# Performance work log

Measured on AMD Instinct MI355X. Metric: run time of the kernel, lower is better.

The kernel has to match this reference:

```python
import jax, jax.numpy as jnp
import numpy as np

B, T, P, HID = 4, 512, 3, 512   # batch, atoms, vector dim, hidden
HD = 32                          # head_dim
H = HID // HD                    # num_heads = 16
EXP = 512                        # expanded (PBC outcell) tokens
S = T + EXP                      # src_len
EPS = 1e-3                       # EquivariantLayerNorm eps
CUTOFF = 1e-5                    # pre-softmax local weight cutoff


def setup_inputs() -> dict:
    key = jax.random.key(0)
    ks = jax.random.split(key, 8)
    q = jax.random.normal(ks[0], (B, T, P, HID), dtype=jnp.float32)
    k = jax.random.normal(ks[1], (B, T, P, HID), dtype=jnp.float32)
    v = jax.random.normal(ks[2], (B, T, P, HID), dtype=jnp.float32)
    attn_bias = jax.random.normal(ks[3], (B, H, T, S), dtype=jnp.float32)
    key_padding_mask = jnp.zeros((B, T), dtype=bool)
    expand_mask = jnp.zeros((B, EXP), dtype=bool)
    outcell_index = jax.random.randint(ks[4], (B, EXP), 0, T)
    local_attention_weight = jax.random.uniform(ks[5], (B, T, S), dtype=jnp.float32)
    out_proj_weight = jax.random.normal(ks[6], (HID, HID), dtype=jnp.float32) / np.sqrt(HID)
    attn_ln_weight = jnp.ones((HID,), dtype=jnp.float32)
    return {"q": q, "k": k, "v": v, "attn_bias": attn_bias,
            "key_padding_mask": key_padding_mask, "outcell_index": outcell_index,
            "local_attention_weight": local_attention_weight, "expand_mask": expand_mask,
            "out_proj_weight": out_proj_weight, "attn_ln_weight": attn_ln_weight}


def _split_heads(x):
    # [b, L, P, HID] -> [b, H, L, P*HD]
    b, L = x.shape[0], x.shape[1]
    return x.reshape(b, L, P, H, HD).transpose(0, 3, 1, 2, 4).reshape(b, H, L, P * HD)


def reference(q, k, v, attn_bias, key_padding_mask, outcell_index,
              local_attention_weight, expand_mask, out_proj_weight, attn_ln_weight):
    # PBC neighbor expansion: gather out-of-cell images of k/v along token dim
    idx = outcell_index[:, :, None, None]  # [B, EXP, 1, 1], broadcast over P, HID
    expand_k = jnp.take_along_axis(k, idx, axis=1)
    expand_v = jnp.take_along_axis(v, idx, axis=1)
    kf = jnp.concatenate([k, expand_k], axis=1)  # [B, S, P, HID]
    vf = jnp.concatenate([v, expand_v], axis=1)
    kpm = jnp.concatenate([key_padding_mask, expand_mask], axis=-1)  # [B, S]

    qh = _split_heads(q)   # [B, H, T, P*HD]
    kh = _split_heads(kf)  # [B, H, S, P*HD]
    vh = _split_heads(vf)

    # attn_bias + key padding mask -> attention mask
    attn_mask = jnp.where(kpm[:, None, None, :], -jnp.inf, attn_bias)
    w = jnp.einsum('bhtd,bhsd->bhts', qh, kh) + attn_mask
    # pre-softmax cutoff where local attention weight is ~0 (use_no_pre_cutoff_softmax=False)
    w = jnp.where((local_attention_weight <= CUTOFF)[:, None, :, :], -jnp.inf, w)
    p = jax.nn.softmax(w.astype(jnp.float32), axis=-1)
    # post-softmax local attention reweighting
    p = p * local_attention_weight[:, None, :, :].astype(jnp.float32)

    attn = jnp.einsum('bhts,bhsd->bhtd', p.astype(q.dtype), vh)  # [B, H, T, P*HD]
    attn = attn.reshape(B, H, T, P, HD).transpose(0, 2, 3, 1, 4).reshape(B, T, P, HID)

    # Equivariant smooth layer norm over the vector dim (-2), mean over width (-1)
    sq = jnp.sum(attn * attn, axis=-2)            # [B, T, HID]
    inv = (jnp.mean(sq, axis=-1) + EPS) ** -0.5   # [B, T]
    xln = attn * attn_ln_weight * inv[:, :, None, None]

    out = jnp.einsum('btpd,od->btpo', xln, out_proj_weight)  # out_proj (no bias)
    return out
```

## Files before the change

### kernel.cpp

```cpp
#include <hip/hip_runtime.h>

#define Bn   4
#define Tn   512
#define Pn   3
#define HIDn 512
#define HDn  32
#define Hn   16
#define EXPn 512
#define Sn   1024
#define Dn   96
#define LOG2E 1.44269504088896340736f

typedef __bf16 bf16_t;
typedef __bf16 bf16x8 __attribute__((ext_vector_type(8)));
typedef float  f32x4  __attribute__((ext_vector_type(4)));

__global__ __launch_bounds__(192) void pack_qk(
    const float* __restrict__ q, const float* __restrict__ k,
    const int* __restrict__ outcell,
    bf16_t* __restrict__ Qh, bf16_t* __restrict__ Kh)
{
    const int bs = blockIdx.x;
    const int b = bs >> 10, s = bs & 1023;
    const int ts = (s < Tn) ? s : outcell[b * EXPn + (s - Tn)];
    const int o = threadIdx.x;
    const int h = o / 12, c = o % 12;
    const int p = c >> 2, f = c & 3;
    const int src = p * HIDn + h * HDn + f * 8;

    {
        const float* krow = k + (size_t)(b * Tn + ts) * (Pn * HIDn);
        const float4* s4 = (const float4*)(krow + src);
        float4 f0 = s4[0], f1 = s4[1];
        bf16_t o8[8] = {(bf16_t)f0.x, (bf16_t)f0.y, (bf16_t)f0.z, (bf16_t)f0.w,
                        (bf16_t)f1.x, (bf16_t)f1.y, (bf16_t)f1.z, (bf16_t)f1.w};
        *(uint4*)&Kh[(((size_t)b * Hn + h) * Sn + s) * Dn + c * 8] = *(uint4*)o8;
    }
    if (s < Tn) {
        const float* qrow = q + (size_t)(b * Tn + s) * (Pn * HIDn);
        const float4* s4 = (const float4*)(qrow + src);
        float4 f0 = s4[0], f1 = s4[1];
        bf16_t o8[8] = {(bf16_t)f0.x, (bf16_t)f0.y, (bf16_t)f0.z, (bf16_t)f0.w,
                        (bf16_t)f1.x, (bf16_t)f1.y, (bf16_t)f1.z, (bf16_t)f1.w};
        *(uint4*)&Qh[(((size_t)b * Hn + h) * Tn + s) * Dn + c * 8] = *(uint4*)o8;
    }
}

__global__ __launch_bounds__(256) void pack_v(
    const float* __restrict__ v, const int* __restrict__ outcell,
    bf16_t* __restrict__ Vt)
{
    const int blk = blockIdx.x;
    const int bh = blk >> 4, s0 = (blk & 15) << 6;
    const int b = bh >> 4, h = bh & 15;
    __shared__ float tile[64 * 108];
    __shared__ int ts_sh[64];
    if (threadIdx.x < 64) {
        const int s = s0 + threadIdx.x;
        ts_sh[threadIdx.x] = (s < Tn) ? s : outcell[b * EXPn + (s - Tn)];
    }
    __syncthreads();
    for (int u = threadIdx.x; u < 64 * 24; u += 256) {
        const int sl = u / 24, c = u % 24;
        const int p = c >> 3, f = c & 7;
        float4 val = *(const float4*)&v[(size_t)(b * Tn + ts_sh[sl]) * (Pn * HIDn)
                                        + p * HIDn + h * HDn + f * 4];
        *(float4*)&tile[sl * 108 + c * 4] = val;
    }
    __syncthreads();
    for (int e = threadIdx.x; e < 96 * 8; e += 256) {
        const int d = e >> 3, g = e & 7;
        bf16_t o8[8];
#pragma unroll
        for (int j = 0; j < 8; ++j) o8[j] = (bf16_t)tile[(g * 8 + j) * 108 + d];
        *(uint4*)&Vt[((size_t)bh * Dn + d) * Sn + s0 + g * 8] = *(uint4*)o8;
    }
}

__global__ __launch_bounds__(256) void pack_w(
    const float* __restrict__ W, bf16_t* __restrict__ Wb)
{
    const int i = blockIdx.x * 256 + threadIdx.x;
    float4 f0 = *(const float4*)&W[i * 8];
    float4 f1 = *(const float4*)&W[i * 8 + 4];
    bf16_t o8[8] = {(bf16_t)f0.x, (bf16_t)f0.y, (bf16_t)f0.z, (bf16_t)f0.w,
                    (bf16_t)f1.x, (bf16_t)f1.y, (bf16_t)f1.z, (bf16_t)f1.w};
    *(uint4*)&Wb[i * 8] = *(uint4*)o8;
}

__global__ __launch_bounds__(256, 2) void attn_kernel(
    const bf16_t* __restrict__ Qh, const bf16_t* __restrict__ Kh,
    const bf16_t* __restrict__ Vt, const float* __restrict__ bias,
    const float* __restrict__ lw, float* __restrict__ attn_out,
    float* __restrict__ sumsq)
{
    const int h  = blockIdx.x;
    const int b  = blockIdx.y >> 3;
    const int t0 = (blockIdx.y & 7) << 6;
    const int tid = threadIdx.x;
    const int wv  = tid >> 6;
    const int lane = tid & 63;
    const int l16 = lane & 15;
    const int quad = lane >> 4;

    __shared__ bf16_t Ps[4][16 * 72];

    const size_t bh = (size_t)b * Hn + h;
    const int tb = t0 + wv * 16;

    bf16x8 qf[3];
    {
        const bf16_t* qb = Qh + (bh * Tn + tb + l16) * Dn + quad * 8;
#pragma unroll
        for (int ks = 0; ks < 3; ++ks) qf[ks] = *(const bf16x8*)(qb + ks * 32);
    }

    const bf16_t* kbase = Kh + (bh * Sn + l16) * Dn + quad * 8;
    const bf16_t* vbase = Vt + (bh * Dn + l16) * Sn + quad * 8;
    const float*  bbase = bias + ((bh * Tn + tb + quad * 4)) * (size_t)Sn + l16;
    const float*  lbase = lw + (((size_t)b * Tn + tb + quad * 4)) * Sn + l16;

    f32x4 Oacc[6];
#pragma unroll
    for (int i = 0; i < 6; ++i) Oacc[i] = f32x4{0.f, 0.f, 0.f, 0.f};
    float mrow[4], lrow[4];
#pragma unroll
    for (int r = 0; r < 4; ++r) { mrow[r] = -3.0e38f; lrow[r] = 0.f; }

    float BRc[16], LRc[16], BRn[16], LRn[16];
#pragma unroll
    for (int ct = 0; ct < 4; ++ct)
#pragma unroll
        for (int r = 0; r < 4; ++r) {
            BRc[ct * 4 + r] = bbase[(size_t)r * Sn + ct * 16];
            LRc[ct * 4 + r] = lbase[(size_t)r * Sn + ct * 16];
        }

    for (int s0 = 0; s0 < Sn; s0 += 64) {
        bf16x8 kf[4][3];
#pragma unroll
        for (int ct = 0; ct < 4; ++ct)
#pragma unroll
            for (int ks = 0; ks < 3; ++ks)
                kf[ct][ks] = *(const bf16x8*)(kbase + (size_t)(s0 + ct * 16) * Dn + ks * 32);

        const int s0n = (s0 + 64 < Sn) ? (s0 + 64) : 0;
#pragma unroll
        for (int ct = 0; ct < 4; ++ct)
#pragma unroll
            for (int r = 0; r < 4; ++r) {
                BRn[ct * 4 + r] = bbase[(size_t)r * Sn + s0n + ct * 16];
                LRn[ct * 4 + r] = lbase[(size_t)r * Sn + s0n + ct * 16];
            }

        f32x4 sc[4];
#pragma unroll
        for (int ct = 0; ct < 4; ++ct) {
            f32x4 acc = f32x4{0.f, 0.f, 0.f, 0.f};
#pragma unroll
            for (int ks = 0; ks < 3; ++ks)
                acc = __builtin_amdgcn_mfma_f32_16x16x32_bf16(qf[ks], kf[ct][ks], acc, 0, 0, 0);
            sc[ct] = acc;
        }

        float cmax[4] = {-3.0e38f, -3.0e38f, -3.0e38f, -3.0e38f};
#pragma unroll
        for (int ct = 0; ct < 4; ++ct) {
#pragma unroll
            for (int r = 0; r < 4; ++r) {
                float wval = sc[ct][r] + BRc[ct * 4 + r];
                wval = (LRc[ct * 4 + r] <= 1e-5f) ? -3.0e38f : wval;
                sc[ct][r] = wval;
                cmax[r] = fmaxf(cmax[r], wval);
            }
        }
#pragma unroll
        for (int off = 1; off < 16; off <<= 1)
#pragma unroll
            for (int r = 0; r < 4; ++r)
                cmax[r] = fmaxf(cmax[r], __shfl_xor(cmax[r], off));

        float scl[4];
#pragma unroll
        for (int r = 0; r < 4; ++r) {
            const float mnew = fmaxf(mrow[r], cmax[r]);
            scl[r] = exp2f((mrow[r] - mnew) * LOG2E);
            mrow[r] = mnew;
            lrow[r] *= scl[r];
        }
#pragma unroll
        for (int dt = 0; dt < 6; ++dt)
#pragma unroll
            for (int r = 0; r < 4; ++r) Oacc[dt][r] *= scl[r];

        float lsum[4] = {0.f, 0.f, 0.f, 0.f};
#pragma unroll
        for (int ct = 0; ct < 4; ++ct) {
#pragma unroll
            for (int r = 0; r < 4; ++r) {
                const float pe = exp2f((sc[ct][r] - mrow[r]) * LOG2E);
                lsum[r] += pe;
                Ps[wv][(quad * 4 + r) * 72 + ct * 16 + l16] = (bf16_t)(pe * LRc[ct * 4 + r]);
            }
        }
#pragma unroll
        for (int off = 1; off < 16; off <<= 1)
#pragma unroll
            for (int r = 0; r < 4; ++r) lsum[r] += __shfl_xor(lsum[r], off);
#pragma unroll
        for (int r = 0; r < 4; ++r) lrow[r] += lsum[r];

        bf16x8 pa[2];
#pragma unroll
        for (int ks = 0; ks < 2; ++ks)
            pa[ks] = *(const bf16x8*)&Ps[wv][l16 * 72 + ks * 32 + quad * 8];
#pragma unroll
        for (int dt = 0; dt < 6; ++dt) {
#pragma unroll
            for (int ks = 0; ks < 2; ++ks) {
                bf16x8 vf = *(const bf16x8*)(vbase + (size_t)(dt * 16) * Sn + s0 + ks * 32);
                Oacc[dt] = __builtin_amdgcn_mfma_f32_16x16x32_bf16(pa[ks], vf, Oacc[dt], 0, 0, 0);
            }
        }

#pragma unroll
        for (int i = 0; i < 16; ++i) { BRc[i] = BRn[i]; LRc[i] = LRn[i]; }
    }

    float invl[4];
#pragma unroll
    for (int r = 0; r < 4; ++r) invl[r] = 1.0f / lrow[r];
    float ss[4] = {0.f, 0.f, 0.f, 0.f};
#pragma unroll
    for (int dt = 0; dt < 6; ++dt) {
        const int d = dt * 16 + l16;
        const int p = d >> 5, hd = d & 31;
#pragma unroll
        for (int r = 0; r < 4; ++r) {
            const int t = tb + quad * 4 + r;
            const float o = Oacc[dt][r] * invl[r];
            attn_out[(((size_t)b * Tn + t) * Pn + p) * HIDn + h * HDn + hd] = o;
            ss[r] += o * o;
        }
    }
#pragma unroll
    for (int off = 1; off < 16; off <<= 1)
#pragma unroll
        for (int r = 0; r < 4; ++r) ss[r] += __shfl_xor(ss[r], off);
    if (l16 == 0) {
#pragma unroll
        for (int r = 0; r < 4; ++r)
            atomicAdd(&sumsq[b * Tn + tb + quad * 4 + r], ss[r]);
    }
}

__global__ __launch_bounds__(256, 2) void out_gemm(
    const float* __restrict__ attn, const float* __restrict__ sumsq,
    const float* __restrict__ lnwg, const bf16_t* __restrict__ Bw,
    float* __restrict__ out)
{
    const int n0 = blockIdx.x * 64;
    const int m0 = blockIdx.y * 64;
    const int tid = threadIdx.x;
    const int wv = tid >> 6, lane = tid & 63, l16 = lane & 15, quad = lane >> 4;
    __shared__ float lnw_s[HIDn];
    __shared__ float inv_s[64];
    __shared__ bf16_t As[2][64 * 72];
    __shared__ bf16_t Bs[2][64 * 72];

    for (int i = tid; i < HIDn; i += 256) lnw_s[i] = lnwg[i];
    if (tid < 64)
        inv_s[tid] = rsqrtf(sumsq[(m0 + tid) / 3] * (1.0f / HIDn) + 1e-3f);
    __syncthreads();

    const int rowA = tid >> 3, cA = tid & 7;
    const float inv0 = inv_s[rowA], inv1 = inv_s[rowA + 32];

    auto loadT = [&](int k0, float4 (&AF)[2][2], uint4 (&BR)[2], float4 (&LF)[2]) {
        LF[0] = *(const float4*)&lnw_s[k0 + cA * 8];
        LF[1] = *(const float4*)&lnw_s[k0 + cA * 8 + 4];
        AF[0][0] = *(const float4*)&attn[(size_t)(m0 + rowA) * HIDn + k0 + cA * 8];
        AF[0][1] = *(const float4*)&attn[(size_t)(m0 + rowA) * HIDn + k0 + cA * 8 + 4];
        AF[1][0] = *(const float4*)&attn[(size_t)(m0 + rowA + 32) * HIDn + k0 + cA * 8];
        AF[1][1] = *(const float4*)&attn[(size_t)(m0 + rowA + 32) * HIDn + k0 + cA * 8 + 4];
        BR[0] = *(const uint4*)&Bw[(size_t)(n0 + rowA) * HIDn + k0 + cA * 8];
        BR[1] = *(const uint4*)&Bw[(size_t)(n0 + rowA + 32) * HIDn + k0 + cA * 8];
    };
    auto storeT = [&](int buf, float4 (&AF)[2][2], uint4 (&BR)[2], float4 (&LF)[2]) {
#pragma unroll
        for (int j = 0; j < 2; ++j) {
            const float iv = j ? inv1 : inv0;
            bf16_t a8[8] = {(bf16_t)(AF[j][0].x * LF[0].x * iv), (bf16_t)(AF[j][0].y * LF[0].y * iv),
                            (bf16_t)(AF[j][0].z * LF[0].z * iv), (bf16_t)(AF[j][0].w * LF[0].w * iv),
                            (bf16_t)(AF[j][1].x * LF[1].x * iv), (bf16_t)(AF[j][1].y * LF[1].y * iv),
                            (bf16_t)(AF[j][1].z * LF[1].z * iv), (bf16_t)(AF[j][1].w * LF[1].w * iv)};
            *(uint4*)&As[buf][(rowA + j * 32) * 72 + cA * 8] = *(uint4*)a8;
            *(uint4*)&Bs[buf][(rowA + j * 32) * 72 + cA * 8] = BR[j];
        }
    };

    f32x4 acc[4];
#pragma unroll
    for (int i = 0; i < 4; ++i) acc[i] = f32x4{0.f, 0.f, 0.f, 0.f};

    float4 af0[2][2], af1[2][2], lf0[2], lf1[2];
    uint4 br0[2], br1[2];
    loadT(0, af0, br0, lf0);
    storeT(0, af0, br0, lf0);
    __syncthreads();

    auto compute = [&](int buf) {
#pragma unroll
        for (int ks = 0; ks < 2; ++ks) {
            bf16x8 a = *(const bf16x8*)&As[buf][(wv * 16 + l16) * 72 + ks * 32 + quad * 8];
#pragma unroll
            for (int nt = 0; nt < 4; ++nt) {
                bf16x8 bb = *(const bf16x8*)&Bs[buf][(nt * 16 + l16) * 72 + ks * 32 + quad * 8];
                acc[nt] = __builtin_amdgcn_mfma_f32_16x16x32_bf16(a, bb, acc[nt], 0, 0, 0);
            }
        }
    };

    for (int it = 0; it < 8; it += 2) {
        loadT((it + 1) * 64, af1, br1, lf1);
        compute(0);
        storeT(1, af1, br1, lf1);
        __syncthreads();
        const bool pf = (it + 2) < 8;
        if (pf) loadT((it + 2) * 64, af0, br0, lf0);
        compute(1);
        if (pf) storeT(0, af0, br0, lf0);
        __syncthreads();
    }
#pragma unroll
    for (int nt = 0; nt < 4; ++nt)
#pragma unroll
        for (int r = 0; r < 4; ++r) {
            const int m = m0 + wv * 16 + quad * 4 + r;
            const int n = n0 + nt * 16 + l16;
            out[(size_t)m * HIDn + n] = acc[nt][r];
        }
}

extern "C" void kernel_launch(void* const* d_in, const int* in_sizes, int n_in,
                              void* d_out, int out_size, void* d_ws, size_t ws_size,
                              hipStream_t stream)
{
    const float* q    = (const float*)d_in[0];
    const float* k    = (const float*)d_in[1];
    const float* v    = (const float*)d_in[2];
    const float* bias = (const float*)d_in[3];
    const int*   outcell = (const int*)d_in[5];
    const float* lw   = (const float*)d_in[6];
    const float* W    = (const float*)d_in[8];
    const float* lnw  = (const float*)d_in[9];
    float* out = (float*)d_out;

    char* ws = (char*)d_ws;
    bf16_t* Qh   = (bf16_t*)(ws);
    bf16_t* Kh   = (bf16_t*)(ws + 6291456);
    bf16_t* Vt   = (bf16_t*)(ws + 18874368);
    float*  attn = (float*)(ws + 31457280);
    bf16_t* Wb   = (bf16_t*)(ws + 44040192);
    float*  sumsq = (float*)(ws + 44564480);

    hipMemsetAsync(sumsq, 0, (Bn * Tn) * sizeof(float), stream);
    pack_qk<<<dim3(Bn * Sn), 192, 0, stream>>>(q, k, outcell, Qh, Kh);
    pack_v<<<dim3(Bn * Hn * 16), 256, 0, stream>>>(v, outcell, Vt);
    pack_w<<<dim3((HIDn * HIDn) / (256 * 8)), 256, 0, stream>>>(W, Wb);
    attn_kernel<<<dim3(Hn, Bn * (Tn / 64)), 256, 0, stream>>>(Qh, Kh, Vt, bias, lw, attn, sumsq);
    out_gemm<<<dim3(HIDn / 64, (Bn * Tn * Pn) / 64), 256, 0, stream>>>(attn, sumsq, lnw, Wb, out);
}
```

Baseline: 344.4 us.

## Stage attention tiles into LDS asynchronously and drop online max rescaling

The attention kernel now streams the K, V, bias and local-weight tiles into double-buffered LDS with global_load_lds, splitting the loads across the four waves and syncing with barriers and vmcnt waits. The chunk size drops to 32 keys. The MFMA operands are swapped so each lane owns one query row, which allows vectorized float4 output stores and simpler reductions. The online softmax running max and rescaling are removed and exp is taken on raw scores, which saves ALU and shuffle work but relies on the scores staying small enough not to overflow.

```diff
diff --git a/kernel.cpp b/kernel.cpp
--- a/kernel.cpp
+++ b/kernel.cpp
@@ -10,10 +10,16 @@
 #define Sn   1024
 #define Dn   96
 #define LOG2E 1.44269504088896340736f
+#define CH   32
+#define NCH  (Sn / CH)
 
 typedef __bf16 bf16_t;
 typedef __bf16 bf16x8 __attribute__((ext_vector_type(8)));
 typedef float  f32x4  __attribute__((ext_vector_type(4)));
+
+#define GLDS(g, l) __builtin_amdgcn_global_load_lds(                            \
+    (const __attribute__((address_space(1))) void*)(g),                         \
+    (__attribute__((address_space(3))) void*)(l), 16, 0, 0)
 
 __global__ __launch_bounds__(192) void pack_qk(
     const float* __restrict__ q, const float* __restrict__ k,
@@ -103,7 +109,11 @@
     const int l16 = lane & 15;
     const int quad = lane >> 4;
 
-    __shared__ bf16_t Ps[4][16 * 72];
+    __shared__ bf16_t KfS[2][6][512];
+    __shared__ bf16_t VfS[2][6][512];
+    __shared__ float  BfS[2][4][2][256];
+    __shared__ float  LfS[2][4][2][256];
+    __shared__ bf16_t Ps[4][16 * 40];
 
     const size_t bh = (size_t)b * Hn + h;
     const int tb = t0 + wv * 16;
@@ -114,144 +124,114 @@
 #pragma unroll
         for (int ks = 0; ks < 3; ++ks) qf[ks] = *(const bf16x8*)(qb + ks * 32);
     }
-
-    const bf16_t* kbase = Kh + (bh * Sn + l16) * Dn + quad * 8;
-    const bf16_t* vbase = Vt + (bh * Dn + l16) * Sn + quad * 8;
-    const float*  bbase = bias + ((bh * Tn + tb + quad * 4)) * (size_t)Sn + l16;
-    const float*  lbase = lw + (((size_t)b * Tn + tb + quad * 4)) * Sn + l16;
+    asm volatile("s_waitcnt vmcnt(0)" ::: "memory");
+
+    int kA, kB, two_k, vA, vB;
+    if (wv == 0)      { kA = 0; kB = 1; two_k = 1; vA = 0; vB = 0; }
+    else if (wv == 1) { kA = 2; kB = 3; two_k = 1; vA = 1; vB = 0; }
+    else if (wv == 2) { kA = 4; kB = 4; two_k = 0; vA = 2; vB = 3; }
+    else              { kA = 5; kB = 5; two_k = 0; vA = 4; vB = 5; }
+
+    const float*  gB = bias + (bh * Tn + tb + l16) * (size_t)Sn + quad * 4;
+    const float*  gL = lw + ((size_t)b * Tn + tb + l16) * Sn + quad * 4;
+    const bf16_t* gKA = Kh + (bh * Sn + (kA / 3) * 16 + l16) * (size_t)Dn + (kA % 3) * 32 + quad * 8;
+    const bf16_t* gKB = Kh + (bh * Sn + (kB / 3) * 16 + l16) * (size_t)Dn + (kB % 3) * 32 + quad * 8;
+    const bf16_t* gVA = Vt + (bh * Dn + vA * 16 + l16) * (size_t)Sn + quad * 8;
+    const bf16_t* gVB = Vt + (bh * Dn + vB * 16 + l16) * (size_t)Sn + quad * 8;
+
+    auto stage = [&](int s0, int buf) {
+        GLDS(gB + s0,      &BfS[buf][wv][0][0]);
+        GLDS(gB + s0 + 16, &BfS[buf][wv][1][0]);
+        GLDS(gL + s0,      &LfS[buf][wv][0][0]);
+        GLDS(gL + s0 + 16, &LfS[buf][wv][1][0]);
+        GLDS(gKA + (size_t)s0 * Dn, &KfS[buf][kA][0]);
+        if (two_k) GLDS(gKB + (size_t)s0 * Dn, &KfS[buf][kB][0]);
+        GLDS(gVA + s0, &VfS[buf][vA][0]);
+        if (!two_k) GLDS(gVB + s0, &VfS[buf][vB][0]);
+    };
 
     f32x4 Oacc[6];
 #pragma unroll
     for (int i = 0; i < 6; ++i) Oacc[i] = f32x4{0.f, 0.f, 0.f, 0.f};
-    float mrow[4], lrow[4];
-#pragma unroll
-    for (int r = 0; r < 4; ++r) { mrow[r] = -3.0e38f; lrow[r] = 0.f; }
-
-    float BRc[16], LRc[16], BRn[16], LRn[16];
-#pragma unroll
-    for (int ct = 0; ct < 4; ++ct)
+    float lacc = 0.f;
+
+    stage(0, 0);
+
+    for (int c = 0; c < NCH; ++c) {
+        const int buf = c & 1;
+        __builtin_amdgcn_sched_barrier(0);
+        __builtin_amdgcn_s_barrier();
+        __builtin_amdgcn_sched_barrier(0);
+        if (c + 1 < NCH) {
+            stage((c + 1) * CH, buf ^ 1);
+            asm volatile("s_waitcnt vmcnt(7)" ::: "memory");
+        } else {
+            asm volatile("s_waitcnt vmcnt(0)" ::: "memory");
+        }
+        __builtin_amdgcn_s_barrier();
+        __builtin_amdgcn_sched_barrier(0);
+
+        f32x4 BR[2], LR[2];
+        BR[0] = *(const f32x4*)&BfS[buf][wv][0][lane * 4];
+        BR[1] = *(const f32x4*)&BfS[buf][wv][1][lane * 4];
+        LR[0] = *(const f32x4*)&LfS[buf][wv][0][lane * 4];
+        LR[1] = *(const f32x4*)&LfS[buf][wv][1][lane * 4];
+
+        f32x4 sc[2];
+#pragma unroll
+        for (int ct = 0; ct < 2; ++ct) {
+            f32x4 acc = f32x4{0.f, 0.f, 0.f, 0.f};
+#pragma unroll
+            for (int ks = 0; ks < 3; ++ks) {
+                bf16x8 kf = *(const bf16x8*)&KfS[buf][ct * 3 + ks][lane * 8];
+                acc = __builtin_amdgcn_mfma_f32_16x16x32_bf16(kf, qf[ks], acc, 0, 0, 0);
+            }
+            sc[ct] = acc;
+        }
+
+        float lsum = 0.f;
+#pragma unroll
+        for (int ct = 0; ct < 2; ++ct) {
+            bf16_t o4[4];
+#pragma unroll
+            for (int r = 0; r < 4; ++r) {
+                const float wval = sc[ct][r] + BR[ct][r];
+                const float pe = (LR[ct][r] <= 1e-5f) ? 0.f : exp2f(wval * LOG2E);
+                lsum += pe;
+                o4[r] = (bf16_t)(pe * LR[ct][r]);
+            }
+            *(uint2*)&Ps[wv][l16 * 40 + ct * 16 + quad * 4] = *(uint2*)o4;
+        }
+        lacc += lsum;
+
+        bf16x8 pb = *(const bf16x8*)&Ps[wv][l16 * 40 + quad * 8];
+#pragma unroll
+        for (int dt = 0; dt < 6; ++dt) {
+            bf16x8 vf = *(const bf16x8*)&VfS[buf][dt][lane * 8];
+            Oacc[dt] = __builtin_amdgcn_mfma_f32_16x16x32_bf16(vf, pb, Oacc[dt], 0, 0, 0);
+        }
+    }
+
+    lacc += __shfl_xor(lacc, 16);
+    lacc += __shfl_xor(lacc, 32);
+    const float invl = 1.0f / lacc;
+    const int t = tb + l16;
+    float ss = 0.f;
+#pragma unroll
+    for (int dt = 0; dt < 6; ++dt) {
+        const int d0 = dt * 16 + quad * 4;
+        f32x4 o;
 #pragma unroll
         for (int r = 0; r < 4; ++r) {
-            BRc[ct * 4 + r] = bbase[(size_t)r * Sn + ct * 16];
-            LRc[ct * 4 + r] = lbase[(size_t)r * Sn + ct * 16];
-        }
-
-    for (int s0 = 0; s0 < Sn; s0 += 64) {
-        bf16x8 kf[4][3];
-#pragma unroll
-        for (int ct = 0; ct < 4; ++ct)
-#pragma unroll
-            for (int ks = 0; ks < 3; ++ks)
-                kf[ct][ks] = *(const bf16x8*)(kbase + (size_t)(s0 + ct * 16) * Dn + ks * 32);
-
-        const int s0n = (s0 + 64 < Sn) ? (s0 + 64) : 0;
-#pragma unroll
-        for (int ct = 0; ct < 4; ++ct)
-#pragma unroll
-            for (int r = 0; r < 4; ++r) {
-                BRn[ct * 4 + r] = bbase[(size_t)r * Sn + s0n + ct * 16];
-                LRn[ct * 4 + r] = lbase[(size_t)r * Sn + s0n + ct * 16];
-            }
-
-        f32x4 sc[4];
-#pragma unroll
-        for (int ct = 0; ct < 4; ++ct) {
-            f32x4 acc = f32x4{0.f, 0.f, 0.f, 0.f};
-#pragma unroll
-            for (int ks = 0; ks < 3; ++ks)
-                acc = __builtin_amdgcn_mfma_f32_16x16x32_bf16(qf[ks], kf[ct][ks], acc, 0, 0, 0);
-            sc[ct] = acc;
-        }
-
-        float cmax[4] = {-3.0e38f, -3.0e38f, -3.0e38f, -3.0e38f};
-#pragma unroll
-        for (int ct = 0; ct < 4; ++ct) {
-#pragma unroll
-            for (int r = 0; r < 4; ++r) {
-                float wval = sc[ct][r] + BRc[ct * 4 + r];
-                wval = (LRc[ct * 4 + r] <= 1e-5f) ? -3.0e38f : wval;
-                sc[ct][r] = wval;
-                cmax[r] = fmaxf(cmax[r], wval);
-            }
-        }
-#pragma unroll
-        for (int off = 1; off < 16; off <<= 1)
-#pragma unroll
-            for (int r = 0; r < 4; ++r)
-                cmax[r] = fmaxf(cmax[r], __shfl_xor(cmax[r], off));
-
-        float scl[4];
-#pragma unroll
-        for (int r = 0; r < 4; ++r) {
-            const float mnew = fmaxf(mrow[r], cmax[r]);
-            scl[r] = exp2f((mrow[r] - mnew) * LOG2E);
-            mrow[r] = mnew;
-            lrow[r] *= scl[r];
-        }
-#pragma unroll
-        for (int dt = 0; dt < 6; ++dt)
-#pragma unroll
-            for (int r = 0; r < 4; ++r) Oacc[dt][r] *= scl[r];
-
-        float lsum[4] = {0.f, 0.f, 0.f, 0.f};
-#pragma unroll
-        for (int ct = 0; ct < 4; ++ct) {
-#pragma unroll
-            for (int r = 0; r < 4; ++r) {
-                const float pe = exp2f((sc[ct][r] - mrow[r]) * LOG2E);
-                lsum[r] += pe;
-                Ps[wv][(quad * 4 + r) * 72 + ct * 16 + l16] = (bf16_t)(pe * LRc[ct * 4 + r]);
-            }
-        }
-#pragma unroll
-        for (int off = 1; off < 16; off <<= 1)
-#pragma unroll
-            for (int r = 0; r < 4; ++r) lsum[r] += __shfl_xor(lsum[r], off);
-#pragma unroll
-        for (int r = 0; r < 4; ++r) lrow[r] += lsum[r];
-
-        bf16x8 pa[2];
-#pragma unroll
-        for (int ks = 0; ks < 2; ++ks)
-            pa[ks] = *(const bf16x8*)&Ps[wv][l16 * 72 + ks * 32 + quad * 8];
-#pragma unroll
-        for (int dt = 0; dt < 6; ++dt) {
-#pragma unroll
-            for (int ks = 0; ks < 2; ++ks) {
-                bf16x8 vf = *(const bf16x8*)(vbase + (size_t)(dt * 16) * Sn + s0 + ks * 32);
-                Oacc[dt] = __builtin_amdgcn_mfma_f32_16x16x32_bf16(pa[ks], vf, Oacc[dt], 0, 0, 0);
-            }
-        }
-
-#pragma unroll
-        for (int i = 0; i < 16; ++i) { BRc[i] = BRn[i]; LRc[i] = LRn[i]; }
-    }
-
-    float invl[4];
-#pragma unroll
-    for (int r = 0; r < 4; ++r) invl[r] = 1.0f / lrow[r];
-    float ss[4] = {0.f, 0.f, 0.f, 0.f};
-#pragma unroll
-    for (int dt = 0; dt < 6; ++dt) {
-        const int d = dt * 16 + l16;
-        const int p = d >> 5, hd = d & 31;
-#pragma unroll
-        for (int r = 0; r < 4; ++r) {
-            const int t = tb + quad * 4 + r;
-            const float o = Oacc[dt][r] * invl[r];
-            attn_out[(((size_t)b * Tn + t) * Pn + p) * HIDn + h * HDn + hd] = o;
-            ss[r] += o * o;
-        }
-    }
-#pragma unroll
-    for (int off = 1; off < 16; off <<= 1)
-#pragma unroll
-        for (int r = 0; r < 4; ++r) ss[r] += __shfl_xor(ss[r], off);
-    if (l16 == 0) {
-#pragma unroll
-        for (int r = 0; r < 4; ++r)
-            atomicAdd(&sumsq[b * Tn + tb + quad * 4 + r], ss[r]);
-    }
+            o[r] = Oacc[dt][r] * invl;
+            ss += o[r] * o[r];
+        }
+        const int p = d0 >> 5, hd = d0 & 31;
+        *(f32x4*)&attn_out[(((size_t)b * Tn + t) * Pn + p) * HIDn + h * HDn + hd] = o;
+    }
+    ss += __shfl_xor(ss, 16);
+    ss += __shfl_xor(ss, 32);
+    if (quad == 0) atomicAdd(&sumsq[b * Tn + t], ss);
 }
 
 __global__ __launch_bounds__(256, 2) void out_gemm(
```

After: 314.3 us. -8.7%, faster.
